# Kernel tuning notes

Hardware: AMD Instinct MI355X
Metric: run time of the kernel (lower is better)

## Reference

```python
import jax, jax.numpy as jnp
import numpy as np


def _params_to_tokens(params):
    # (batch, 2k) -> (batch, k, 2) : chunk into freqs/amps then stack
    freqs, amps = jnp.split(params, 2, axis=-1)
    return jnp.stack((freqs, amps), axis=-1)


def setup_inputs() -> dict:
    key = jax.random.key(0)
    k1, k2 = jax.random.split(key)
    predicted = jax.random.normal(k1, (64, 4096), dtype=jnp.float32)
    target = jax.random.normal(k2, (64, 4096), dtype=jnp.float32)
    return {"predicted": predicted, "target": target}


def reference(predicted, target):
    p = _params_to_tokens(predicted)   # (b, k, 2)
    t = _params_to_tokens(target)      # (b, k, 2)
    # Euclidean cdist via gram-matrix identity (avoids (b,k,k,2) broadcast temp)
    p2 = jnp.sum(p * p, axis=-1)       # (b, k)
    t2 = jnp.sum(t * t, axis=-1)       # (b, k)
    gram = jnp.einsum('bid,bjd->bij', p, t)  # (b, k, k)
    sq = p2[:, :, None] + t2[:, None, :] - 2.0 * gram
    costs = jnp.sqrt(jnp.maximum(sq, 0.0))   # (b, k, k)
    min1 = jnp.mean(jnp.min(costs, axis=1), axis=-1)  # min over predicted dim
    min2 = jnp.mean(jnp.min(costs, axis=2), axis=-1)  # min over target dim
    return jnp.mean(min1 + min2)
```

## Files before the change

kernel.cpp:

```cpp
#include <hip/hip_runtime.h>


typedef float v2f __attribute__((ext_vector_type(2)));

__device__ __forceinline__ float min3f(float a, float b, float c) {
  float d;
  asm("v_min3_f32 %0, %1, %2, %3" : "=v"(d) : "v"(a), "v"(b), "v"(c));
  return d;
}

constexpr int K = 2048;
constexpr int BLOCK = 256;
constexpr int Q = 8;
constexpr int S = 8;
constexpr int QT = 32;
constexpr int JT = K / S;
constexpr unsigned INF_U = 0x7F800000u;

__global__ __launch_bounds__(BLOCK, 4) void chamfer_kernel(
    const float* __restrict__ pred, const float* __restrict__ targ,
    float* __restrict__ out) {
  const int tile = blockIdx.x;
  const int b    = blockIdx.y;
  const int dir  = blockIdx.z;

  const float* qbase = (dir == 0 ? pred : targ) + (size_t)b * (2 * K);
  const float* obase = (dir == 0 ? targ : pred) + (size_t)b * (2 * K);

  const int tid = threadIdx.x;
  const int t   = tid & (QT - 1);
  const int s   = tid >> 5;

  __shared__ float4   smem4[K / 2];
  __shared__ unsigned rowmin_u[BLOCK];
  __shared__ float    wsum[BLOCK / 64];

  {
    const float2* o2 = (const float2*)obase;
    #pragma unroll
    for (int i = tid; i < K / 2; i += BLOCK) {
      const float2 xx = o2[i];
      const float2 yy = o2[(K / 2) + i];
      smem4[i] = make_float4(xx.x, xx.y, yy.x, yy.y);
    }
    rowmin_u[tid] = INF_U;
  }

  v2f nxv[Q], nyv[Q];
  float p2[Q], mins[Q];
  #pragma unroll
  for (int q = 0; q < Q; ++q) {
    const int qi = tile * (QT * Q) + q * QT + t;
    const float px = qbase[qi];
    const float py = qbase[K + qi];
    nxv[q].x = -2.0f * px; nxv[q].y = -2.0f * px;
    nyv[q].x = -2.0f * py; nyv[q].y = -2.0f * py;
    p2[q]   = fmaf(px, px, py * py);
    mins[q] = 3.4e38f;
  }
  __syncthreads();

  const float4* sbase = smem4 + s * (JT / 2);
  #pragma unroll 4
  for (int j2 = 0; j2 < JT / 2; ++j2) {
    const float4 a = sbase[j2];
    v2f xs; xs.x = a.x; xs.y = a.y;
    v2f ys; ys.x = a.z; ys.y = a.w;
    const v2f t2 = __builtin_elementwise_fma(ys, ys, xs * xs);
    #pragma unroll
    for (int q = 0; q < Q; ++q) {
      const v2f sc = __builtin_elementwise_fma(
          nyv[q], ys, __builtin_elementwise_fma(nxv[q], xs, t2));
      mins[q] = min3f(sc.x, sc.y, mins[q]);
    }
  }

  #pragma unroll
  for (int q = 0; q < Q; ++q) {
    const float cand = fmaxf(mins[q] + p2[q], 0.0f);
    atomicMin(&rowmin_u[q * QT + t], __float_as_uint(cand));
  }
  __syncthreads();

  float v = sqrtf(__uint_as_float(rowmin_u[tid]));
  #pragma unroll
  for (int off = 32; off; off >>= 1) v += __shfl_down(v, off, 64);
  const int lane = tid & 63, w = tid >> 6;
  if (lane == 0) wsum[w] = v;
  __syncthreads();
  if (w == 0) {
    float sum = (lane < BLOCK / 64) ? wsum[lane] : 0.0f;
    #pragma unroll
    for (int off = 2; off; off >>= 1) sum += __shfl_down(sum, off, 64);
    if (lane == 0) atomicAdd(out, sum * (1.0f / 131072.0f));
  }
}

extern "C" void kernel_launch(void* const* d_in, const int* in_sizes, int n_in,
                              void* d_out, int out_size, void* d_ws, size_t ws_size,
                              hipStream_t stream) {
  const float* pred = (const float*)d_in[0];
  const float* targ = (const float*)d_in[1];
  float* out = (float*)d_out;

  dim3 grid(K / (QT * Q), 64, 2);
  chamfer_kernel<<<grid, dim3(BLOCK), 0, stream>>>(pred, targ, out);
}
```

Measured before the change: 87.68 us.

## Halve queries per block and double target splits, add LDS prefetch

```diff
diff --git a/kernel.cpp b/kernel.cpp
--- a/kernel.cpp
+++ b/kernel.cpp
@@ -12,9 +12,10 @@
 constexpr int K = 2048;
 constexpr int BLOCK = 256;
 constexpr int Q = 8;
-constexpr int S = 8;
-constexpr int QT = 32;
+constexpr int QT = 16;
+constexpr int S = 16;
 constexpr int JT = K / S;
+constexpr int NQB = QT * Q;
 constexpr unsigned INF_U = 0x7F800000u;
 
 __global__ __launch_bounds__(BLOCK, 4) void chamfer_kernel(
@@ -29,10 +30,10 @@
 
   const int tid = threadIdx.x;
   const int t   = tid & (QT - 1);
-  const int s   = tid >> 5;
+  const int s   = tid >> 4;
 
   __shared__ float4   smem4[K / 2];
-  __shared__ unsigned rowmin_u[BLOCK];
+  __shared__ unsigned rowmin_u[NQB];
   __shared__ float    wsum[BLOCK / 64];
 
   {
@@ -43,14 +44,14 @@
       const float2 yy = o2[(K / 2) + i];
       smem4[i] = make_float4(xx.x, xx.y, yy.x, yy.y);
     }
-    rowmin_u[tid] = INF_U;
+    if (tid < NQB) rowmin_u[tid] = INF_U;
   }
 
   v2f nxv[Q], nyv[Q];
   float p2[Q], mins[Q];
   #pragma unroll
   for (int q = 0; q < Q; ++q) {
-    const int qi = tile * (QT * Q) + q * QT + t;
+    const int qi = tile * NQB + q * QT + t;
     const float px = qbase[qi];
     const float py = qbase[K + qi];
     nxv[q].x = -2.0f * px; nxv[q].y = -2.0f * px;
@@ -61,9 +62,7 @@
   __syncthreads();
 
   const float4* sbase = smem4 + s * (JT / 2);
-  #pragma unroll 4
-  for (int j2 = 0; j2 < JT / 2; ++j2) {
-    const float4 a = sbase[j2];
+  auto body = [&](const float4 a) {
     v2f xs; xs.x = a.x; xs.y = a.y;
     v2f ys; ys.x = a.z; ys.y = a.w;
     const v2f t2 = __builtin_elementwise_fma(ys, ys, xs * xs);
@@ -73,7 +72,18 @@
           nyv[q], ys, __builtin_elementwise_fma(nxv[q], xs, t2));
       mins[q] = min3f(sc.x, sc.y, mins[q]);
     }
+  };
+  float4 a0 = sbase[0];
+  float4 a1 = sbase[1];
+  #pragma unroll 2
+  for (int j2 = 0; j2 < JT / 2 - 2; ++j2) {
+    const float4 an = sbase[j2 + 2];
+    body(a0);
+    a0 = a1;
+    a1 = an;
   }
+  body(a0);
+  body(a1);
 
   #pragma unroll
   for (int q = 0; q < Q; ++q) {
@@ -82,17 +92,14 @@
   }
   __syncthreads();
 
-  float v = sqrtf(__uint_as_float(rowmin_u[tid]));
+  float v = (tid < NQB) ? sqrtf(__uint_as_float(rowmin_u[tid])) : 0.0f;
   #pragma unroll
   for (int off = 32; off; off >>= 1) v += __shfl_down(v, off, 64);
   const int lane = tid & 63, w = tid >> 6;
   if (lane == 0) wsum[w] = v;
   __syncthreads();
-  if (w == 0) {
-    float sum = (lane < BLOCK / 64) ? wsum[lane] : 0.0f;
-    #pragma unroll
-    for (int off = 2; off; off >>= 1) sum += __shfl_down(sum, off, 64);
-    if (lane == 0) atomicAdd(out, sum * (1.0f / 131072.0f));
+  if (tid == 0) {
+    atomicAdd(out, (wsum[0] + wsum[1] + wsum[2] + wsum[3]) * (1.0f / 131072.0f));
   }
 }
 
@@ -103,6 +110,6 @@
   const float* targ = (const float*)d_in[1];
   float* out = (float*)d_out;
 
-  dim3 grid(K / (QT * Q), 64, 2);
+  dim3 grid(K / NQB, 64, 2);
   chamfer_kernel<<<grid, dim3(BLOCK), 0, stream>>>(pred, targ, out);
 }
```

After: 90.25 us. 2.9% more time.
